# Kernel tuning notes

Measured on AMD Instinct MI355X. Metric: run time of the kernel, lower is better.

Reference implementation:

```python
import jax, jax.numpy as jnp
import numpy as np

BS = 1
H_ = 200
W_ = 200
NQ = H_ * W_          # 40000 BEV queries == num_value
D = 256
NH = 8
DH = D // NH          # 32
NL = 1
NP = 4
NQUEUE = 2
B2 = BS * NQUEUE


def setup_inputs() -> dict:
    key = jax.random.key(0)
    ks = jax.random.split(key, 12)
    s = 0.02
    inp = {
        "query": jax.random.normal(ks[0], (BS, NQ, D), jnp.float32),
        "query_pos": jax.random.normal(ks[1], (BS, NQ, D), jnp.float32) * 0.1,
        "reference_points": jax.random.uniform(ks[2], (BS, NQ, NL, 2), jnp.float32),
        # sampling_offsets linear: in = d_model*num_bev_queue, out = queue*heads*levels*points*2
        "W_so": jax.random.normal(ks[3], (D * NQUEUE, NQUEUE * NH * NL * NP * 2), jnp.float32) * s,
        "b_so": jax.random.normal(ks[4], (NQUEUE * NH * NL * NP * 2,), jnp.float32),
        # attention_weights linear: out = queue*heads*levels*points
        "W_aw": jax.random.normal(ks[5], (D * NQUEUE, NQUEUE * NH * NL * NP), jnp.float32) * s,
        "b_aw": jax.random.normal(ks[6], (NQUEUE * NH * NL * NP,), jnp.float32) * s,
        "W_v": jax.random.normal(ks[7], (D, D), jnp.float32) * s,
        "b_v": jax.random.normal(ks[8], (D,), jnp.float32) * s,
        "W_o": jax.random.normal(ks[9], (D, D), jnp.float32) * s,
        "b_o": jax.random.normal(ks[10], (D,), jnp.float32) * s,
    }
    return inp


def _deform_attn_single_level(v, loc, attn_w):
    """v: (B, Nv, NH, DH); loc: (B, Nq, NH, NP, 2) in [0,1]; attn_w: (B, Nq, NH, NP).
    grid_sample semantics: align_corners=False, zero padding."""
    B = v.shape[0]
    vt = v.transpose(0, 2, 1, 3)                      # (B, NH, Nv, DH)
    # pixel coords (align_corners=False): p = loc * size - 0.5
    x = (loc[..., 0] * W_ - 0.5).transpose(0, 2, 1, 3).reshape(B, NH, -1)  # (B, NH, Nq*NP)
    y = (loc[..., 1] * H_ - 0.5).transpose(0, 2, 1, 3).reshape(B, NH, -1)
    wt = attn_w.transpose(0, 2, 1, 3).reshape(B, NH, -1)
    x0f = jnp.floor(x); y0f = jnp.floor(y)
    x0 = x0f.astype(jnp.int32); y0 = y0f.astype(jnp.int32)
    x1 = x0 + 1; y1 = y0 + 1
    wx1 = x - x0f; wx0 = 1.0 - wx1
    wy1 = y - y0f; wy0 = 1.0 - wy1

    def corner(ix, iy, cw):
        valid = (ix >= 0) & (ix < W_) & (iy >= 0) & (iy < H_)
        idx = jnp.clip(iy, 0, H_ - 1) * W_ + jnp.clip(ix, 0, W_ - 1)
        g = jnp.take_along_axis(vt, idx[..., None], axis=2)   # (B, NH, Nq*NP, DH)
        return g * (cw * valid.astype(cw.dtype))[..., None]

    acc = (corner(x0, y0, wx0 * wy0) + corner(x1, y0, wx1 * wy0)
           + corner(x0, y1, wx0 * wy1) + corner(x1, y1, wx1 * wy1))
    acc = acc * wt[..., None]
    acc = acc.reshape(B, NH, -1, NP, DH).sum(3)               # (B, NH, Nq, DH)
    return acc.transpose(0, 2, 1, 3).reshape(B, -1, NH * DH)  # (B, Nq, D)


def reference(query, query_pos, reference_points, W_so, b_so, W_aw, b_aw, W_v, b_v, W_o, b_o):
    # input_flatten defaults to query (pre-positional); query gets pos added
    q = query + query_pos
    # default queue construction: duplicate current BEV -> (bs*queue, Nv, D)
    value = jnp.stack([query, query], axis=1).reshape(B2, NQ, D)
    history_bev = value[:BS]                                   # (bs, Nv, D)
    qwh = jnp.concatenate([history_bev, q], axis=-1)           # (bs, Nq, 2D)
    # value projection
    v = (value @ W_v + b_v).reshape(B2, NQ, NH, DH)
    # offsets / weights from concatenated features
    so = (qwh @ W_so + b_so).reshape(BS, NQ, NH, NQUEUE, NL, NP, 2)
    aw = (qwh @ W_aw + b_aw).reshape(BS, NQ, NH, NQUEUE, NL * NP)
    aw = jax.nn.softmax(aw, axis=-1).reshape(BS, NQ, NH, NQUEUE, NL, NP)
    aw = aw.transpose(0, 3, 1, 2, 4, 5).reshape(B2, NQ, NH, NL, NP)
    so = so.transpose(0, 3, 1, 2, 4, 5, 6).reshape(B2, NQ, NH, NL, NP, 2)
    # duplicate reference points across the queue
    rp = jnp.stack([reference_points] * NQUEUE, axis=1).reshape(B2, NQ, NL, 2)
    offset_norm = jnp.array([W_, H_], jnp.float32)             # (w, h)
    loc = rp[:, :, None, :, None, :] + so / offset_norm        # (B2, NQ, NH, NL, NP, 2)
    out = _deform_attn_single_level(v, loc[:, :, :, 0], aw[:, :, :, 0])  # (B2, NQ, D)
    # fuse queue outputs by mean (queue is the fast axis of B2)
    out = out.reshape(BS, NQUEUE, NQ, D).mean(axis=1)
    return out @ W_o + b_o
```

## Files before the change

kernel.cpp:

```cpp
#include <hip/hip_runtime.h>
#include <math.h>

#define NQc 40000
#define Wc 200
#define Hc 200

typedef __attribute__((ext_vector_type(8))) short short8;
typedef __attribute__((ext_vector_type(4))) float f32x4;
typedef __attribute__((ext_vector_type(2))) float f32x2;

#define VMWAIT(N) asm volatile("s_waitcnt vmcnt(" #N ")" ::: "memory")

__device__ __forceinline__ ushort f2b(float f) {
  unsigned u = __float_as_uint(f);
  u = (u + 0x7fffu + ((u >> 16) & 1u)) >> 16;
  return (ushort)u;
}

__device__ __forceinline__ void glds16(const void* g, void* l) {
  __builtin_amdgcn_global_load_lds(
      (const __attribute__((address_space(1))) void*)g,
      (__attribute__((address_space(3))) void*)l, 16, 0, 0);
}

__global__ __launch_bounds__(256) void prep_w(
    const float* __restrict__ Wv, const float* __restrict__ Wo,
    const float* __restrict__ Wso, const float* __restrict__ Waw,
    ushort* __restrict__ WvT, ushort* __restrict__ WoT,
    ushort* __restrict__ WsoT, ushort* __restrict__ WawT) {
  const int idx = blockIdx.x * 256 + threadIdx.x;
  if (idx < 65536) {
    int n = idx >> 8, k = idx & 255;
    WvT[idx] = f2b(Wv[k * 256 + n]);
  } else if (idx < 131072) {
    int i = idx - 65536;
    int n = i >> 8, k = i & 255;
    WoT[i] = f2b(Wo[k * 256 + n]);
  } else if (idx < 196608) {
    int i = idx - 131072;
    int n = i >> 9, k = i & 511;
    WsoT[i] = f2b(Wso[k * 128 + n]);
  } else {
    int i = idx - 196608;
    int n = i >> 9, k = i & 511;
    WawT[i] = f2b(Waw[k * 64 + n]);
  }
}

__global__ __launch_bounds__(256, 1) void fused_front(
    const float* __restrict__ q, const float* __restrict__ qp,
    const ushort* __restrict__ WvT, const ushort* __restrict__ WsoT,
    const ushort* __restrict__ WawT,
    const float* __restrict__ bv, const float* __restrict__ b_so,
    const float* __restrict__ b_aw,
    ushort* __restrict__ vt, float* __restrict__ so_ws,
    float* __restrict__ aw_ws) {
  __shared__ __align__(16) char smem[131072];
  ushort* Ab = (ushort*)smem;
  float (*E)[68] = (float(*)[68])(smem + 65536);
  ushort (*Eb)[72] = (ushort(*)[72])(smem + 65536);
  f32x4 vacc[16] = {};
  f32x4 sacc[12] = {};
  const int m0 = blockIdx.x * 64;
  const int tid = threadIdx.x;
  const int w = tid >> 6, lane = tid & 63;
  const int rl = lane & 15, q2 = lane >> 4;
  const int sw8 = rl & 7;
  const int lrow = lane >> 3, lch = (lane & 7) ^ (lrow & 7);

  {
    const int arow = tid >> 2, qn = tid & 3;
    const float* qr  = q  + (size_t)(m0 + arow) * 256 + qn * 64;
    const float* qpr = qp + (size_t)(m0 + arow) * 256 + qn * 64;
    ushort* Alo = Ab + arow * 256;
    ushort* Ahi = Ab + 16384 + arow * 256;
    const int swz = arow & 7;
#pragma unroll
    for (int i = 0; i < 4; ++i) {
      float4 a[4], p[4];
#pragma unroll
      for (int k = 0; k < 4; ++k) a[k] = *(const float4*)(qr + i * 16 + k * 4);
#pragma unroll
      for (int k = 0; k < 4; ++k) p[k] = *(const float4*)(qpr + i * 16 + k * 4);
      ushort lo[16], hi[16];
#pragma unroll
      for (int k = 0; k < 4; ++k) {
        lo[k * 4 + 0] = f2b(a[k].x); lo[k * 4 + 1] = f2b(a[k].y);
        lo[k * 4 + 2] = f2b(a[k].z); lo[k * 4 + 3] = f2b(a[k].w);
        hi[k * 4 + 0] = f2b(a[k].x + p[k].x); hi[k * 4 + 1] = f2b(a[k].y + p[k].y);
        hi[k * 4 + 2] = f2b(a[k].z + p[k].z); hi[k * 4 + 3] = f2b(a[k].w + p[k].w);
      }
      const int cb = qn * 8 + i * 2;
      *(uint4*)&Alo[(cb ^ swz) * 8]       = *(const uint4*)&lo[0];
      *(uint4*)&Alo[((cb + 1) ^ swz) * 8] = *(const uint4*)&lo[8];
      *(uint4*)&Ahi[(cb ^ swz) * 8]       = *(const uint4*)&hi[0];
      *(uint4*)&Ahi[((cb + 1) ^ swz) * 8] = *(const uint4*)&hi[8];
    }
  }
  __syncthreads();

  auto STAGEV = [&](int buf, int t) {
    ushort* Bs = (ushort*)(smem + 65536 + buf * 32768);
    const int k0 = t * 64;
#pragma unroll
    for (int i = 0; i < 8; ++i) {
      const int g = w * 8 + i;
      const int row = g * 8 + lrow;
      glds16(WvT + (size_t)row * 256 + k0 + lch * 8, Bs + g * 512 + lane * 8);
    }
  };
  auto STAGES = [&](int buf, int s) {
    ushort* Bs = (ushort*)(smem + 65536 + buf * 32768);
    const int k0 = s * 64;
#pragma unroll
    for (int i = 0; i < 6; ++i) {
      const int g = w * 6 + i;
      const int row = g * 8 + lrow;
      const ushort* src = (row < 128)
          ? WsoT + (size_t)row * 512 + k0 + lch * 8
          : WawT + (size_t)(row - 128) * 512 + k0 + lch * 8;
      glds16(src, Bs + g * 512 + lane * 8);
    }
  };

  STAGEV(0, 0);
#pragma unroll
  for (int u = 0; u < 12; ++u) {
    if (u < 3)        { STAGEV((u + 1) & 1, u + 1); VMWAIT(8); }
    else if (u == 3)  { STAGES(0, 0);               VMWAIT(6); }
    else if (u < 11)  { STAGES((u + 1) & 1, u - 3); VMWAIT(6); }
    else              { VMWAIT(0); }
    __builtin_amdgcn_s_barrier();
    const ushort* Bs = (const ushort*)(smem + 65536 + (u & 1) * 32768);
    if (u < 4) {
#pragma unroll
      for (int kk = 0; kk < 2; ++kk) {
        const short8 af = *(const short8*)
            &Ab[(w * 16 + rl) * 256 + ((u * 8 + kk * 4 + q2) ^ sw8) * 8];
#pragma unroll
        for (int nj = 0; nj < 16; ++nj) {
          const short8 bf = *(const short8*)
              &Bs[(nj * 16 + rl) * 64 + ((kk * 4 + q2) ^ sw8) * 8];
          vacc[nj] = __builtin_amdgcn_mfma_f32_16x16x32_bf16(af, bf, vacc[nj], 0, 0, 0);
        }
      }
    } else {
      const int s = u - 4, sel = s >> 2, tl = s & 3;
#pragma unroll
      for (int kk = 0; kk < 2; ++kk) {
        const short8 af = *(const short8*)
            &Ab[sel * 16384 + (w * 16 + rl) * 256 +
                ((tl * 8 + kk * 4 + q2) ^ sw8) * 8];
#pragma unroll
        for (int nj = 0; nj < 12; ++nj) {
          const short8 bf = *(const short8*)
              &Bs[(nj * 16 + rl) * 64 + ((kk * 4 + q2) ^ sw8) * 8];
          sacc[nj] = __builtin_amdgcn_mfma_f32_16x16x32_bf16(af, bf, sacc[nj], 0, 0, 0);
        }
      }
    }
    __builtin_amdgcn_s_barrier();
  }

  const int rbase = q2 * 4, cl = rl;

#pragma unroll
  for (int p4 = 0; p4 < 4; ++p4) {
#pragma unroll
    for (int j = 0; j < 4; ++j) {
      const int nj = p4 * 4 + j;
      const int n = p4 * 64 + j * 16 + cl;
      const float bb = bv[n];
      const f32x4 a = vacc[nj];
#pragma unroll
      for (int r = 0; r < 4; ++r)
        Eb[w * 16 + rbase + r][j * 16 + cl] = f2b(a[r] + bb);
    }
    __syncthreads();
#pragma unroll
    for (int hh = 0; hh < 2; ++hh) {
      const int h = p4 * 2 + hh;
#pragma unroll
      for (int it = 0; it < 2; ++it) {
        const int flat = it * 256 + tid;
        const int row = flat >> 3, d4 = (flat & 7) * 4;
        *(ushort4*)&vt[((size_t)h * NQc + m0 + row) * 32 + d4] =
            *(const ushort4*)&Eb[row][hh * 32 + d4];
      }
    }
    __syncthreads();
  }

#pragma unroll
  for (int p = 0; p < 3; ++p) {
#pragma unroll
    for (int j = 0; j < 4; ++j) {
      const int nj = p * 4 + j;
      const int nl = j * 16 + cl;
      const f32x4 a = sacc[nj];
      if (p < 2) {
        const float bb = b_so[p * 64 + nl];
#pragma unroll
        for (int r = 0; r < 4; ++r)
          E[w * 16 + rbase + r][nl] = a[r] + bb;
      } else {
        const float bb = b_aw[nl];
#pragma unroll
        for (int r = 0; r < 4; ++r) {
          float z = a[r] + bb;
          float zm = fmaxf(z, __shfl_xor(z, 1, 64));
          zm = fmaxf(zm, __shfl_xor(zm, 2, 64));
          float e = expf(z - zm);
          float s = e + __shfl_xor(e, 1, 64);
          s = s + __shfl_xor(s, 2, 64);
          E[w * 16 + rbase + r][nl] = e / s;
        }
      }
    }
    __syncthreads();
#pragma unroll
    for (int it = 0; it < 4; ++it) {
      const int flat = it * 256 + tid;
      const int row = flat >> 4, c4 = (flat & 15) * 4;
      const float4 vle = *(const float4*)&E[row][c4];
      if (p < 2)
        *(float4*)&so_ws[(size_t)(m0 + row) * 128 + p * 64 + c4] = vle;
      else
        *(float4*)&aw_ws[(size_t)(m0 + row) * 64 + c4] = vle;
    }
    __syncthreads();
  }
}

__global__ __launch_bounds__(256, 3) void gemm_o_k(
    const ushort* __restrict__ Ap, const ushort* __restrict__ WoT,
    const float* __restrict__ bo, float* __restrict__ out) {
  __shared__ __align__(16) char smem[49152];
  float (*E)[68] = (float(*)[68])smem;
  f32x4 acc[8] = {};
  const int m0 = blockIdx.x * 64, n0 = blockIdx.y * 128;
  const int tid = threadIdx.x;
  const int w = tid >> 6, lane = tid & 63;
  const int rl = lane & 15, q2 = lane >> 4;
  const int sw8 = rl & 7;
  const int lrow = lane >> 3, lch = (lane & 7) ^ (lrow & 7);

  auto STAGE = [&](int buf, int t) {
    ushort* As = (ushort*)(smem + buf * 24576);
    ushort* Bs = As + 4096;
    const int k0 = t * 64;
#pragma unroll
    for (int i = 0; i < 2; ++i) {
      const int g = w * 2 + i;
      const int row = g * 8 + lrow;
      glds16(Ap + (size_t)(m0 + row) * 256 + k0 + lch * 8,
             As + g * 512 + lane * 8);
    }
#pragma unroll
    for (int i = 0; i < 4; ++i) {
      const int g = w * 4 + i;
      const int row = g * 8 + lrow;
      glds16(WoT + (size_t)(n0 + row) * 256 + k0 + lch * 8,
             Bs + g * 512 + lane * 8);
    }
  };

  STAGE(0, 0);
#pragma unroll
  for (int t = 0; t < 4; ++t) {
    const int cur = t & 1;
    if (t < 3) {
      STAGE(cur ^ 1, t + 1);
      VMWAIT(6);
    } else {
      VMWAIT(0);
    }
    __builtin_amdgcn_s_barrier();
    {
      const ushort* Asb = (const ushort*)(smem + cur * 24576);
      const ushort* Bsb = Asb + 4096;
#pragma unroll
      for (int kk = 0; kk < 2; ++kk) {
        const short8 af = *(const short8*)
            &Asb[(w * 16 + rl) * 64 + ((kk * 4 + q2) ^ sw8) * 8];
#pragma unroll
        for (int nj = 0; nj < 8; ++nj) {
          const short8 bf = *(const short8*)
              &Bsb[(nj * 16 + rl) * 64 + ((kk * 4 + q2) ^ sw8) * 8];
          acc[nj] = __builtin_amdgcn_mfma_f32_16x16x32_bf16(af, bf, acc[nj], 0, 0, 0);
        }
      }
    }
    __builtin_amdgcn_s_barrier();
  }

  const int rbase = q2 * 4, cl = rl;
#pragma unroll
  for (int p = 0; p < 2; ++p) {
#pragma unroll
    for (int j = 0; j < 4; ++j) {
      const int nj = p * 4 + j;
      const int n = n0 + p * 64 + j * 16 + cl;
      const float bb = bo[n];
      const f32x4 a = acc[nj];
#pragma unroll
      for (int r = 0; r < 4; ++r)
        E[w * 16 + rbase + r][j * 16 + cl] = a[r] + bb;
    }
    __syncthreads();
#pragma unroll
    for (int it = 0; it < 4; ++it) {
      const int flat = it * 256 + tid;
      const int row = flat >> 4, c4 = (flat & 15) * 4;
      *(float4*)&out[(size_t)(m0 + row) * 256 + n0 + p * 64 + c4] =
          *(const float4*)&E[row][c4];
    }
    __syncthreads();
  }
}

__global__ __launch_bounds__(256) void sample_kernel(
    const ushort* __restrict__ vt,
    const float* __restrict__ so_ws,
    const float* __restrict__ aw_ws,
    const float* __restrict__ refp,
    ushort* __restrict__ out_pre)
{
  __shared__ int2   offs[32][9];
  __shared__ float2 wts2[32][9][2];
  const int h  = blockIdx.x & 7;
  const int m0 = (blockIdx.x >> 3) * 32;
  const int tid = threadIdx.x;

  {
    const int j  = tid & 7;
    const int qi = tid >> 3;
    const int m  = m0 + qi;
    const int c  = h * 8 + j;
    const float sx  = so_ws[(size_t)m * 128 + c * 2 + 0];
    const float sy  = so_ws[(size_t)m * 128 + c * 2 + 1];
    const float wgt = 0.5f * aw_ws[(size_t)m * 64 + c];
    const float x = refp[m * 2 + 0] * (float)Wc + sx - 0.5f;
    const float y = refp[m * 2 + 1] * (float)Hc + sy - 0.5f;
    const float x0f = floorf(x), y0f = floorf(y);
    const int x0 = (int)x0f, y0 = (int)y0f;
    const int x1 = x0 + 1, y1 = y0 + 1;
    const float wx1 = x - x0f, wx0 = 1.0f - wx1;
    const float wy1 = y - y0f, wy0 = 1.0f - wy1;
    const float wx0v = (x0 >= 0 && x0 < Wc) ? wx0 : 0.0f;
    const float wx1v = (x1 >= 0 && x1 < Wc) ? wx1 : 0.0f;
    const float wy0v = ((y0 >= 0 && y0 < Hc) ? wy0 : 0.0f) * wgt;
    const float wy1v = ((y1 >= 0 && y1 < Hc) ? wy1 : 0.0f) * wgt;
    const int bx = min(max(x0, 0), Wc - 2);
    const float wl = (bx == x0) ? wx0v : ((bx == x1) ? wx1v : 0.0f);
    const float wr = (bx + 1 == x1) ? wx1v : ((bx + 1 == x0) ? wx0v : 0.0f);
    const int cy0 = min(max(y0, 0), Hc - 1);
    const int cy1 = min(max(y1, 0), Hc - 1);
    offs[qi][j] = make_int2((cy0 * Wc + bx) * 64, (cy1 * Wc + bx) * 64);
    wts2[qi][j][0] = make_float2(wl * wy0v, wl * wy1v);
    wts2[qi][j][1] = make_float2(wr * wy0v, wr * wy1v);
  }
  __syncthreads();

  const int qi = tid >> 3;
  const int ld = tid & 7;
  const int m  = m0 + qi;
  const int hf = ld >> 2;
  const char* __restrict__ vb =
      (const char*)(vt + (size_t)h * NQc * 32) + (uint)(ld * 16);

  uint4 raw[16];
#pragma unroll
  for (int j = 0; j < 8; ++j) {
    const int2 oo = offs[qi][j];
    raw[2 * j]     = *(const uint4*)(vb + (uint)oo.x);
    raw[2 * j + 1] = *(const uint4*)(vb + (uint)oo.y);
  }
  __builtin_amdgcn_sched_barrier(0);

  f32x2 acc0 = {0.0f, 0.0f}, acc1 = {0.0f, 0.0f};
  f32x2 acc2 = {0.0f, 0.0f}, acc3 = {0.0f, 0.0f};

#pragma unroll
  for (int j = 0; j < 8; ++j) {
    const float2 wp = wts2[qi][j][hf];
#pragma unroll
    for (int r = 0; r < 2; ++r) {
      const uint4 rawv = raw[2 * j + r];
      const float w = (r == 0) ? wp.x : wp.y;
      const f32x2 wv = {w, w};
      f32x2 v0, v1, v2, v3;
      v0.x = __uint_as_float(rawv.x << 16);
      v0.y = __uint_as_float(rawv.x & 0xFFFF0000u);
      v1.x = __uint_as_float(rawv.y << 16);
      v1.y = __uint_as_float(rawv.y & 0xFFFF0000u);
      v2.x = __uint_as_float(rawv.z << 16);
      v2.y = __uint_as_float(rawv.z & 0xFFFF0000u);
      v3.x = __uint_as_float(rawv.w << 16);
      v3.y = __uint_as_float(rawv.w & 0xFFFF0000u);
#if __has_builtin(__builtin_elementwise_fma)
      acc0 = __builtin_elementwise_fma(wv, v0, acc0);
      acc1 = __builtin_elementwise_fma(wv, v1, acc1);
      acc2 = __builtin_elementwise_fma(wv, v2, acc2);
      acc3 = __builtin_elementwise_fma(wv, v3, acc3);
#else
      acc0.x = fmaf(w, v0.x, acc0.x); acc0.y = fmaf(w, v0.y, acc0.y);
      acc1.x = fmaf(w, v1.x, acc1.x); acc1.y = fmaf(w, v1.y, acc1.y);
      acc2.x = fmaf(w, v2.x, acc2.x); acc2.y = fmaf(w, v2.y, acc2.y);
      acc3.x = fmaf(w, v3.x, acc3.x); acc3.y = fmaf(w, v3.y, acc3.y);
#endif
    }
  }

  float a[8] = {acc0.x, acc0.y, acc1.x, acc1.y,
                acc2.x, acc2.y, acc3.x, acc3.y};
#pragma unroll
  for (int k = 0; k < 8; ++k) a[k] += __shfl_xor(a[k], 4, 64);

  if (hf == 0) {
    ushort rr[8];
#pragma unroll
    for (int k = 0; k < 8; ++k) rr[k] = f2b(a[k]);
    *(uint4*)&out_pre[(size_t)m * 256 + h * 32 + ld * 8] = *(const uint4*)rr;
  }
}

extern "C" void kernel_launch(void* const* d_in, const int* in_sizes, int n_in,
                              void* d_out, int out_size, void* d_ws, size_t ws_size,
                              hipStream_t stream) {
  const float* query     = (const float*)d_in[0];
  const float* query_pos = (const float*)d_in[1];
  const float* refp      = (const float*)d_in[2];
  const float* W_so      = (const float*)d_in[3];
  const float* b_so      = (const float*)d_in[4];
  const float* W_aw      = (const float*)d_in[5];
  const float* b_aw      = (const float*)d_in[6];
  const float* W_v       = (const float*)d_in[7];
  const float* b_v       = (const float*)d_in[8];
  const float* W_o       = (const float*)d_in[9];
  const float* b_o       = (const float*)d_in[10];
  float* out = (float*)d_out;

  char* base = (char*)d_ws;
  ushort* vt      = (ushort*)base;
  float*  so_ws   = (float*)(base + 20480000);
  float*  aw_ws   = (float*)(base + 40960000);
  ushort* out_pre = (ushort*)(base + 51200000);
  ushort* WvT     = (ushort*)(base + 71680000);
  ushort* WoT     = WvT + 65536;
  ushort* WsoT    = WoT + 65536;
  ushort* WawT    = WsoT + 65536;

  prep_w<<<896, 256, 0, stream>>>(W_v, W_o, W_so, W_aw, WvT, WoT, WsoT, WawT);
  fused_front<<<625, 256, 0, stream>>>(query, query_pos, WvT, WsoT, WawT,
                                       b_v, b_so, b_aw, vt, so_ws, aw_ws);
  sample_kernel<<<10000, 256, 0, stream>>>(vt, so_ws, aw_ws, refp, out_pre);
  gemm_o_k<<<dim3(625, 2), 256, 0, stream>>>(out_pre, WoT, b_o, out);
}
```

Before: 237.6 us.

## Load GEMM operands directly from global memory instead of LDS staging

Both the fused front GEMM and the output GEMM drop their LDS double-buffered staging (global_load_lds with waitcnt pipelining). Each lane now reads its A and B MFMA fragments straight from global memory, and LDS shrinks to only the epilogue buffer. Occupancy bounds rise to 3 and 4 blocks per CU. The goal is to remove barriers and LDS pressure and to allow more concurrent blocks. The cost is that weight fragments are re-read from global/L2 by every wave, with uncoalesced 16-byte strided accesses and no software prefetch.

Measured after the change: 425.2 us. 78.9% more time.

```diff
diff --git a/kernel.cpp b/kernel.cpp
--- a/kernel.cpp
+++ b/kernel.cpp
@@ -8,19 +8,11 @@
 typedef __attribute__((ext_vector_type(8))) short short8;
 typedef __attribute__((ext_vector_type(4))) float f32x4;
 typedef __attribute__((ext_vector_type(2))) float f32x2;
-
-#define VMWAIT(N) asm volatile("s_waitcnt vmcnt(" #N ")" ::: "memory")
 
 __device__ __forceinline__ ushort f2b(float f) {
   unsigned u = __float_as_uint(f);
   u = (u + 0x7fffu + ((u >> 16) & 1u)) >> 16;
   return (ushort)u;
-}
-
-__device__ __forceinline__ void glds16(const void* g, void* l) {
-  __builtin_amdgcn_global_load_lds(
-      (const __attribute__((address_space(1))) void*)g,
-      (__attribute__((address_space(3))) void*)l, 16, 0, 0);
 }
 
 __global__ __launch_bounds__(256) void prep_w(
@@ -47,7 +39,7 @@
   }
 }
 
-__global__ __launch_bounds__(256, 1) void fused_front(
+__global__ __launch_bounds__(256, 3) void fused_front(
     const float* __restrict__ q, const float* __restrict__ qp,
     const ushort* __restrict__ WvT, const ushort* __restrict__ WsoT,
     const ushort* __restrict__ WawT,
@@ -55,117 +47,79 @@
     const float* __restrict__ b_aw,
     ushort* __restrict__ vt, float* __restrict__ so_ws,
     float* __restrict__ aw_ws) {
-  __shared__ __align__(16) char smem[131072];
-  ushort* Ab = (ushort*)smem;
-  float (*E)[68] = (float(*)[68])(smem + 65536);
-  ushort (*Eb)[72] = (ushort(*)[72])(smem + 65536);
+  __shared__ __align__(16) char smem[17408];
+  float (*E)[68] = (float(*)[68])smem;
+  ushort (*Eb)[72] = (ushort(*)[72])smem;
   f32x4 vacc[16] = {};
   f32x4 sacc[12] = {};
   const int m0 = blockIdx.x * 64;
   const int tid = threadIdx.x;
   const int w = tid >> 6, lane = tid & 63;
   const int rl = lane & 15, q2 = lane >> 4;
-  const int sw8 = rl & 7;
-  const int lrow = lane >> 3, lch = (lane & 7) ^ (lrow & 7);
-
-  {
-    const int arow = tid >> 2, qn = tid & 3;
-    const float* qr  = q  + (size_t)(m0 + arow) * 256 + qn * 64;
-    const float* qpr = qp + (size_t)(m0 + arow) * 256 + qn * 64;
-    ushort* Alo = Ab + arow * 256;
-    ushort* Ahi = Ab + 16384 + arow * 256;
-    const int swz = arow & 7;
-#pragma unroll
-    for (int i = 0; i < 4; ++i) {
-      float4 a[4], p[4];
-#pragma unroll
-      for (int k = 0; k < 4; ++k) a[k] = *(const float4*)(qr + i * 16 + k * 4);
-#pragma unroll
-      for (int k = 0; k < 4; ++k) p[k] = *(const float4*)(qpr + i * 16 + k * 4);
-      ushort lo[16], hi[16];
-#pragma unroll
-      for (int k = 0; k < 4; ++k) {
-        lo[k * 4 + 0] = f2b(a[k].x); lo[k * 4 + 1] = f2b(a[k].y);
-        lo[k * 4 + 2] = f2b(a[k].z); lo[k * 4 + 3] = f2b(a[k].w);
-        hi[k * 4 + 0] = f2b(a[k].x + p[k].x); hi[k * 4 + 1] = f2b(a[k].y + p[k].y);
-        hi[k * 4 + 2] = f2b(a[k].z + p[k].z); hi[k * 4 + 3] = f2b(a[k].w + p[k].w);
-      }
-      const int cb = qn * 8 + i * 2;
-      *(uint4*)&Alo[(cb ^ swz) * 8]       = *(const uint4*)&lo[0];
-      *(uint4*)&Alo[((cb + 1) ^ swz) * 8] = *(const uint4*)&lo[8];
-      *(uint4*)&Ahi[(cb ^ swz) * 8]       = *(const uint4*)&hi[0];
-      *(uint4*)&Ahi[((cb + 1) ^ swz) * 8] = *(const uint4*)&hi[8];
-    }
-  }
-  __syncthreads();
-
-  auto STAGEV = [&](int buf, int t) {
-    ushort* Bs = (ushort*)(smem + 65536 + buf * 32768);
-    const int k0 = t * 64;
-#pragma unroll
-    for (int i = 0; i < 8; ++i) {
-      const int g = w * 8 + i;
-      const int row = g * 8 + lrow;
-      glds16(WvT + (size_t)row * 256 + k0 + lch * 8, Bs + g * 512 + lane * 8);
-    }
-  };
-  auto STAGES = [&](int buf, int s) {
-    ushort* Bs = (ushort*)(smem + 65536 + buf * 32768);
-    const int k0 = s * 64;
-#pragma unroll
-    for (int i = 0; i < 6; ++i) {
-      const int g = w * 6 + i;
-      const int row = g * 8 + lrow;
-      const ushort* src = (row < 128)
-          ? WsoT + (size_t)row * 512 + k0 + lch * 8
-          : WawT + (size_t)(row - 128) * 512 + k0 + lch * 8;
-      glds16(src, Bs + g * 512 + lane * 8);
-    }
-  };
-
-  STAGEV(0, 0);
-#pragma unroll
-  for (int u = 0; u < 12; ++u) {
-    if (u < 3)        { STAGEV((u + 1) & 1, u + 1); VMWAIT(8); }
-    else if (u == 3)  { STAGES(0, 0);               VMWAIT(6); }
-    else if (u < 11)  { STAGES((u + 1) & 1, u - 3); VMWAIT(6); }
-    else              { VMWAIT(0); }
-    __builtin_amdgcn_s_barrier();
-    const ushort* Bs = (const ushort*)(smem + 65536 + (u & 1) * 32768);
-    if (u < 4) {
-#pragma unroll
-      for (int kk = 0; kk < 2; ++kk) {
-        const short8 af = *(const short8*)
-            &Ab[(w * 16 + rl) * 256 + ((u * 8 + kk * 4 + q2) ^ sw8) * 8];
-#pragma unroll
-        for (int nj = 0; nj < 16; ++nj) {
-          const short8 bf = *(const short8*)
-              &Bs[(nj * 16 + rl) * 64 + ((kk * 4 + q2) ^ sw8) * 8];
-          vacc[nj] = __builtin_amdgcn_mfma_f32_16x16x32_bf16(af, bf, vacc[nj], 0, 0, 0);
-        }
-      }
-    } else {
-      const int s = u - 4, sel = s >> 2, tl = s & 3;
-#pragma unroll
-      for (int kk = 0; kk < 2; ++kk) {
-        const short8 af = *(const short8*)
-            &Ab[sel * 16384 + (w * 16 + rl) * 256 +
-                ((tl * 8 + kk * 4 + q2) ^ sw8) * 8];
-#pragma unroll
-        for (int nj = 0; nj < 12; ++nj) {
-          const short8 bf = *(const short8*)
-              &Bs[(nj * 16 + rl) * 64 + ((kk * 4 + q2) ^ sw8) * 8];
-          sacc[nj] = __builtin_amdgcn_mfma_f32_16x16x32_bf16(af, bf, sacc[nj], 0, 0, 0);
-        }
-      }
-    }
-    __builtin_amdgcn_s_barrier();
+  const int row = w * 16 + rl;
+
+  const float*  qA  = q  + (size_t)(m0 + row) * 256 + q2 * 8;
+  const float*  qpA = qp + (size_t)(m0 + row) * 256 + q2 * 8;
+  const ushort* BV  = WvT  + (size_t)rl * 256 + q2 * 8;
+  const ushort* BS  = WsoT + (size_t)rl * 512 + q2 * 8;
+  const ushort* BA  = WawT + (size_t)rl * 512 + q2 * 8;
+
+#pragma unroll
+  for (int t = 0; t < 4; ++t) {
+#pragma unroll
+    for (int kk = 0; kk < 2; ++kk) {
+      const int ko = t * 64 + kk * 32;
+      const float4 a0 = *(const float4*)(qA + ko);
+      const float4 a1 = *(const float4*)(qA + ko + 4);
+      ushort u[8];
+      u[0] = f2b(a0.x); u[1] = f2b(a0.y); u[2] = f2b(a0.z); u[3] = f2b(a0.w);
+      u[4] = f2b(a1.x); u[5] = f2b(a1.y); u[6] = f2b(a1.z); u[7] = f2b(a1.w);
+      const short8 af = *(const short8*)u;
+#pragma unroll
+      for (int nj = 0; nj < 16; ++nj) {
+        const short8 bf = *(const short8*)(BV + nj * 4096 + ko);
+        vacc[nj] = __builtin_amdgcn_mfma_f32_16x16x32_bf16(af, bf, vacc[nj], 0, 0, 0);
+      }
+#pragma unroll
+      for (int nj = 0; nj < 12; ++nj) {
+        const short8 bf = (nj < 8)
+            ? *(const short8*)(BS + nj * 8192 + ko)
+            : *(const short8*)(BA + (nj - 8) * 8192 + ko);
+        sacc[nj] = __builtin_amdgcn_mfma_f32_16x16x32_bf16(af, bf, sacc[nj], 0, 0, 0);
+      }
+    }
+  }
+#pragma unroll
+  for (int t = 4; t < 8; ++t) {
+#pragma unroll
+    for (int kk = 0; kk < 2; ++kk) {
+      const int ko = t * 64 + kk * 32;
+      const int ka = ko - 256;
+      const float4 a0 = *(const float4*)(qA + ka);
+      const float4 a1 = *(const float4*)(qA + ka + 4);
+      const float4 p0 = *(const float4*)(qpA + ka);
+      const float4 p1 = *(const float4*)(qpA + ka + 4);
+      ushort u[8];
+      u[0] = f2b(a0.x + p0.x); u[1] = f2b(a0.y + p0.y);
+      u[2] = f2b(a0.z + p0.z); u[3] = f2b(a0.w + p0.w);
+      u[4] = f2b(a1.x + p1.x); u[5] = f2b(a1.y + p1.y);
+      u[6] = f2b(a1.z + p1.z); u[7] = f2b(a1.w + p1.w);
+      const short8 af = *(const short8*)u;
+#pragma unroll
+      for (int nj = 0; nj < 12; ++nj) {
+        const short8 bf = (nj < 8)
+            ? *(const short8*)(BS + nj * 8192 + ko)
+            : *(const short8*)(BA + (nj - 8) * 8192 + ko);
+        sacc[nj] = __builtin_amdgcn_mfma_f32_16x16x32_bf16(af, bf, sacc[nj], 0, 0, 0);
+      }
+    }
   }
 
   const int rbase = q2 * 4, cl = rl;
 
 #pragma unroll
   for (int p4 = 0; p4 < 4; ++p4) {
+    __syncthreads();
 #pragma unroll
     for (int j = 0; j < 4; ++j) {
       const int nj = p4 * 4 + j;
@@ -183,16 +137,16 @@
 #pragma unroll
       for (int it = 0; it < 2; ++it) {
         const int flat = it * 256 + tid;
-        const int row = flat >> 3, d4 = (flat & 7) * 4;
-        *(ushort4*)&vt[((size_t)h * NQc + m0 + row) * 32 + d4] =
-            *(const ushort4*)&Eb[row][hh * 32 + d4];
-      }
-    }
-    __syncthreads();
+        const int erow = flat >> 3, d4 = (flat & 7) * 4;
+        *(ushort4*)&vt[((size_t)h * NQc + m0 + erow) * 32 + d4] =
+            *(const ushort4*)&Eb[erow][hh * 32 + d4];
+      }
+    }
   }
 
 #pragma unroll
   for (int p = 0; p < 3; ++p) {
+    __syncthreads();
 #pragma unroll
     for (int j = 0; j < 4; ++j) {
       const int nj = p * 4 + j;
@@ -221,82 +175,49 @@
 #pragma unroll
     for (int it = 0; it < 4; ++it) {
       const int flat = it * 256 + tid;
-      const int row = flat >> 4, c4 = (flat & 15) * 4;
-      const float4 vle = *(const float4*)&E[row][c4];
+      const int erow = flat >> 4, c4 = (flat & 15) * 4;
+      const float4 vle = *(const float4*)&E[erow][c4];
       if (p < 2)
-        *(float4*)&so_ws[(size_t)(m0 + row) * 128 + p * 64 + c4] = vle;
+        *(float4*)&so_ws[(size_t)(m0 + erow) * 128 + p * 64 + c4] = vle;
       else
-        *(float4*)&aw_ws[(size_t)(m0 + row) * 64 + c4] = vle;
-    }
-    __syncthreads();
-  }
-}
-
-__global__ __launch_bounds__(256, 3) void gemm_o_k(
+        *(float4*)&aw_ws[(size_t)(m0 + erow) * 64 + c4] = vle;
+    }
+  }
+}
+
+__global__ __launch_bounds__(256, 4) void gemm_o_k(
     const ushort* __restrict__ Ap, const ushort* __restrict__ WoT,
     const float* __restrict__ bo, float* __restrict__ out) {
-  __shared__ __align__(16) char smem[49152];
+  __shared__ __align__(16) char smem[17408];
   float (*E)[68] = (float(*)[68])smem;
   f32x4 acc[8] = {};
   const int m0 = blockIdx.x * 64, n0 = blockIdx.y * 128;
   const int tid = threadIdx.x;
   const int w = tid >> 6, lane = tid & 63;
   const int rl = lane & 15, q2 = lane >> 4;
-  const int sw8 = rl & 7;
-  const int lrow = lane >> 3, lch = (lane & 7) ^ (lrow & 7);
-
-  auto STAGE = [&](int buf, int t) {
-    ushort* As = (ushort*)(smem + buf * 24576);
-    ushort* Bs = As + 4096;
-    const int k0 = t * 64;
-#pragma unroll
-    for (int i = 0; i < 2; ++i) {
-      const int g = w * 2 + i;
-      const int row = g * 8 + lrow;
-      glds16(Ap + (size_t)(m0 + row) * 256 + k0 + lch * 8,
-             As + g * 512 + lane * 8);
-    }
-#pragma unroll
-    for (int i = 0; i < 4; ++i) {
-      const int g = w * 4 + i;
-      const int row = g * 8 + lrow;
-      glds16(WoT + (size_t)(n0 + row) * 256 + k0 + lch * 8,
-             Bs + g * 512 + lane * 8);
-    }
-  };
-
-  STAGE(0, 0);
+  const int row = w * 16 + rl;
+
+  const ushort* A0 = Ap + (size_t)(m0 + row) * 256 + q2 * 8;
+  const ushort* B0 = WoT + (size_t)(n0 + rl) * 256 + q2 * 8;
+
 #pragma unroll
   for (int t = 0; t < 4; ++t) {
-    const int cur = t & 1;
-    if (t < 3) {
-      STAGE(cur ^ 1, t + 1);
-      VMWAIT(6);
-    } else {
-      VMWAIT(0);
-    }
-    __builtin_amdgcn_s_barrier();
-    {
-      const ushort* Asb = (const ushort*)(smem + cur * 24576);
-      const ushort* Bsb = Asb + 4096;
-#pragma unroll
-      for (int kk = 0; kk < 2; ++kk) {
-        const short8 af = *(const short8*)
-            &Asb[(w * 16 + rl) * 64 + ((kk * 4 + q2) ^ sw8) * 8];
-#pragma unroll
-        for (int nj = 0; nj < 8; ++nj) {
-          const short8 bf = *(const short8*)
-              &Bsb[(nj * 16 + rl) * 64 + ((kk * 4 + q2) ^ sw8) * 8];
-          acc[nj] = __builtin_amdgcn_mfma_f32_16x16x32_bf16(af, bf, acc[nj], 0, 0, 0);
-        }
-      }
-    }
-    __builtin_amdgcn_s_barrier();
+#pragma unroll
+    for (int kk = 0; kk < 2; ++kk) {
+      const int ko = t * 64 + kk * 32;
+      const short8 af = *(const short8*)(A0 + ko);
+#pragma unroll
+      for (int nj = 0; nj < 8; ++nj) {
+        const short8 bf = *(const short8*)(B0 + nj * 4096 + ko);
+        acc[nj] = __builtin_amdgcn_mfma_f32_16x16x32_bf16(af, bf, acc[nj], 0, 0, 0);
+      }
+    }
   }
 
   const int rbase = q2 * 4, cl = rl;
 #pragma unroll
   for (int p = 0; p < 2; ++p) {
+    __syncthreads();
 #pragma unroll
     for (int j = 0; j < 4; ++j) {
       const int nj = p * 4 + j;
@@ -311,11 +232,10 @@
 #pragma unroll
     for (int it = 0; it < 4; ++it) {
       const int flat = it * 256 + tid;
-      const int row = flat >> 4, c4 = (flat & 15) * 4;
-      *(float4*)&out[(size_t)(m0 + row) * 256 + n0 + p * 64 + c4] =
-          *(const float4*)&E[row][c4];
-    }
-    __syncthreads();
+      const int erow = flat >> 4, c4 = (flat & 15) * 4;
+      *(float4*)&out[(size_t)(m0 + erow) * 256 + n0 + p * 64 + c4] =
+          *(const float4*)&E[erow][c4];
+    }
   }
 }
 
```
